# Performance work log

Hardware: AMD Instinct MI355X
Metric: run time of the kernel (lower is better)

## Reference

```python
import jax, jax.numpy as jnp
import numpy as np


def setup_inputs() -> dict:
    key = jax.random.key(0)
    k1, k2 = jax.random.split(key)
    B, T, C = 16, 4096, 128
    unary_logits = jax.random.normal(k1, (B, T, C), dtype=jnp.float32)
    log_trans = jax.random.normal(k2, (C, C), dtype=jnp.float32)
    return {"unary_logits": unary_logits, "log_trans": log_trans}


def reference(unary_logits, log_trans):
    # Row-normalized log transition matrix (log_softmax over dim=1)
    lt = jax.nn.log_softmax(log_trans, axis=1)  # (C, C)
    B, T, C = unary_logits.shape
    u = jnp.swapaxes(unary_logits, 0, 1)  # (T, B, C) time-major for scan

    # Forward recursion: alpha_t = u_t + logsumexp_i(alpha_{t-1}[i] + lt[i, j])
    def fwd_step(a_prev, u_t):
        a_new = u_t + jax.nn.logsumexp(a_prev[:, :, None] + lt[None, :, :], axis=1)
        return a_new, a_new

    a0 = u[0]
    _, alphas_rest = jax.lax.scan(fwd_step, a0, u[1:])
    alpha = jnp.concatenate([a0[None], alphas_rest], axis=0)  # (T, B, C)

    # Backward recursion: beta_t = logsumexp_j(beta_{t+1}[j] + u_{t+1}[j] + lt[i, j])
    def bwd_step(b_next, u_next):
        b_new = jax.nn.logsumexp(
            b_next[:, None, :] + u_next[:, None, :] + lt[None, :, :], axis=2
        )
        return b_new, b_new

    bT = jnp.zeros((B, C), dtype=u.dtype)
    _, betas_rest = jax.lax.scan(bwd_step, bT, u[1:], reverse=True)
    beta = jnp.concatenate([betas_rest, bT[None]], axis=0)  # (T, B, C)

    log_marginals = alpha + beta
    out = jax.nn.log_softmax(log_marginals, axis=-1)
    return jnp.swapaxes(out, 0, 1)  # (B, T, C)
```

## Files before the change

kernel.cpp:

```cpp
#include <hip/hip_runtime.h>
#include <math.h>

#define BB 16
#define TT 4096
#define CC 128

#define LCH 32
#define WCH 48
#define NCH (TT / LCH)

#define ERS 132

typedef float    f32x4  __attribute__((ext_vector_type(4)));
typedef unsigned uint4v __attribute__((ext_vector_type(4)));
typedef __bf16   bf16x8 __attribute__((ext_vector_type(8)));


__device__ __forceinline__ float wave_reduce_max(float v) {
#pragma unroll
    for (int o = 1; o < 64; o <<= 1) v = fmaxf(v, __shfl_xor(v, o, 64));
    return v;
}
__device__ __forceinline__ float wave_reduce_sum(float v) {
#pragma unroll
    for (int o = 1; o < 64; o <<= 1) v += __shfl_xor(v, o, 64);
    return v;
}

__device__ __forceinline__ void lds_barrier() {
    __asm__ __volatile__("s_waitcnt lgkmcnt(0)" ::: "memory");
    __builtin_amdgcn_s_barrier();
}

__device__ __forceinline__ unsigned pkbf(float f) {
    unsigned u = __float_as_uint(f);
    float hi = __uint_as_float(u & 0xffff0000u);
    float lo = f - hi;
    return (u >> 16) | (__float_as_uint(lo) & 0xffff0000u);
}

__global__ __launch_bounds__(CC) void prep_kernel(const float* __restrict__ lt,
                                                  unsigned short* __restrict__ fr) {
    const int r  = blockIdx.x;
    const int j  = threadIdx.x;
    const int wv = j >> 6;
    __shared__ float sm[2];

    float x = lt[r * CC + j];
    float m = wave_reduce_max(x);
    if ((j & 63) == 0) sm[wv] = m;
    __syncthreads();
    m = fmaxf(sm[0], sm[1]);
    __syncthreads();
    float e = __expf(x - m);
    float s = wave_reduce_sum(e);
    if ((j & 63) == 0) sm[wv] = s;
    __syncthreads();
    s = sm[0] + sm[1];
    float p = e / s;

    unsigned pk = pkbf(p);
    unsigned short phi = (unsigned short)(pk & 0xffffu);
    unsigned short plo = (unsigned short)(pk >> 16);

    {
        int T = j >> 4, col = j & 15, kc = r >> 5;
        int ln = (((r & 31) >> 3) << 4) | col, e8 = r & 7;
        size_t o = ((((size_t)(0 * 8 + T) * 4 + kc) * 2 + 0) * 64 + ln) * 8 + e8;
        fr[o] = phi; fr[o + 512] = plo;
    }
    {
        int T = r >> 4, col = r & 15, kc = j >> 5;
        int ln = (((j & 31) >> 3) << 4) | col, e8 = j & 7;
        size_t o = ((((size_t)(1 * 8 + T) * 4 + kc) * 2 + 0) * 64 + ln) * 8 + e8;
        fr[o] = phi; fr[o + 512] = plo;
    }
}

#define BDECL()                                                                \
    bf16x8 Bh_0, Bh_1, Bh_2, Bh_3, Bl_0, Bl_1, Bl_2, Bl_3

#define BLOAD(kc)                                                              \
    do {                                                                       \
        size_t o = ((((size_t)(dirIdx * 8 + wv) * 4 + (kc)) * 2)               \
                        * 64 + lane) * 8;                                      \
        Bh_##kc = __builtin_bit_cast(bf16x8, *(const uint4v*)(fr + o));        \
        Bl_##kc =                                                              \
            __builtin_bit_cast(bf16x8, *(const uint4v*)(fr + o + 512));        \
    } while (0)

#define KC_STEP(kc)                                                            \
    do {                                                                       \
        const uint4v* eptr = (const uint4v*)(epar + arow + (kc) * 32);         \
        uint4v w0 = eptr[0], w1 = eptr[1];                                     \
        uint4v ahw, alw;                                                       \
        ahw.x = __builtin_amdgcn_perm(w0.y, w0.x, 0x05040100u);                \
        ahw.y = __builtin_amdgcn_perm(w0.w, w0.z, 0x05040100u);                \
        ahw.z = __builtin_amdgcn_perm(w1.y, w1.x, 0x05040100u);                \
        ahw.w = __builtin_amdgcn_perm(w1.w, w1.z, 0x05040100u);                \
        alw.x = __builtin_amdgcn_perm(w0.y, w0.x, 0x07060302u);                \
        alw.y = __builtin_amdgcn_perm(w0.w, w0.z, 0x07060302u);                \
        alw.z = __builtin_amdgcn_perm(w1.y, w1.x, 0x07060302u);                \
        alw.w = __builtin_amdgcn_perm(w1.w, w1.z, 0x07060302u);                \
        bf16x8 Ah = __builtin_bit_cast(bf16x8, ahw);                           \
        bf16x8 Al = __builtin_bit_cast(bf16x8, alw);                           \
        accHH = __builtin_amdgcn_mfma_f32_16x16x32_bf16(Ah, Bh_##kc, accHH, 0, 0, 0); \
        accHL = __builtin_amdgcn_mfma_f32_16x16x32_bf16(Ah, Bl_##kc, accHL, 0, 0, 0); \
        accLH = __builtin_amdgcn_mfma_f32_16x16x32_bf16(Al, Bh_##kc, accLH, 0, 0, 0); \
    } while (0)

#define LOADU(d0, ROW)                                                         \
    do {                                                                       \
        size_t ro = (size_t)(ROW) * CC;                                        \
        d0.x = ub0[ro + n1]; d0.y = ub1[ro + n1];                              \
        d0.z = ub2[ro + n1]; d0.w = ub3[ro + n1];                              \
    } while (0)

#define STOREO(s0, ROW)                                                        \
    do {                                                                       \
        size_t ro = (size_t)(ROW) * CC;                                        \
        ob0[ro + n1] = s0.x; ob1[ro + n1] = s0.y;                              \
        ob2[ro + n1] = s0.z; ob3[ro + n1] = s0.w;                              \
    } while (0)

__global__ __launch_bounds__(512, 1)
void scan_kernel(const float* __restrict__ u,
                 const unsigned short* __restrict__ fr,
                 float* __restrict__ alpha,
                 float* __restrict__ beta) {
    const int t    = threadIdx.x;
    const int lane = t & 63;
    const int wv   = t >> 6;
    const int col  = lane & 15;
    const int bb   = (lane >> 4) * 4;
    const int n1   = wv * 16 + col;

    const int  id     = blockIdx.x;
    const bool fwd    = id < NCH;
    const int  c      = fwd ? id : id - NCH;
    const int  dirIdx = fwd ? 0 : 1;

    __shared__ alignas(16) unsigned Epk[2][16 * ERS];
    __shared__ alignas(16) float    wpub[2][16];

    BDECL();
    BLOAD(0); BLOAD(1); BLOAD(2); BLOAD(3);

    const float* ub0 = u + (size_t)(bb + 0) * TT * CC;
    const float* ub1 = u + (size_t)(bb + 1) * TT * CC;
    const float* ub2 = u + (size_t)(bb + 2) * TT * CC;
    const float* ub3 = u + (size_t)(bb + 3) * TT * CC;
    float* obase = fwd ? alpha : beta;
    float* ob0 = obase + (size_t)(bb + 0) * TT * CC;
    float* ob1 = obase + (size_t)(bb + 1) * TT * CC;
    float* ob2 = obase + (size_t)(bb + 2) * TT * CC;
    float* ob3 = obase + (size_t)(bb + 3) * TT * CC;

    const int wlo = c * LCH;
    const int whi = wlo + LCH;
    int t0 = 0, t1 = 0, NS;
    if (fwd) {
        t0 = wlo - WCH; if (t0 < 0) t0 = 0;
        NS = whi - 1 - t0;
    } else {
        t1 = whi - 1 + WCH; if (t1 > TT - 1) t1 = TT - 1;
        NS = t1 - wlo;
    }

    float4 x0, uc0, un0;
    if (fwd) {
        LOADU(x0, t0);
        if (t0 == 0 && wlo == 0) STOREO(x0, 0);
    } else {
        LOADU(x0, t1);
        if (t1 == whi - 1) {
            float4 z4{0.f, 0.f, 0.f, 0.f};
            STOREO(z4, t1);
        }
    }
    {
        int tr0 = fwd ? (t0 + 1) : (t1 - 1);
        LOADU(un0, tr0);
    }
    if (wv == 0 && col == 0) {
        *(float4*)&wpub[0][bb] = x0;
        *(float4*)&wpub[1][bb] = x0;
    }
    lds_barrier();

    const int arow = (lane & 15) * ERS + (lane >> 4) * 8;

    for (int s = 0; s < NS; ++s) {
        const int par = s & 1;
        unsigned* epar = &Epk[par][0];

        float4 wmy = *(const float4*)&wpub[par][bb];
        epar[(bb + 0) * ERS + n1] = pkbf(__expf(x0.x - wmy.x));
        epar[(bb + 1) * ERS + n1] = pkbf(__expf(x0.y - wmy.y));
        epar[(bb + 2) * ERS + n1] = pkbf(__expf(x0.z - wmy.z));
        epar[(bb + 3) * ERS + n1] = pkbf(__expf(x0.w - wmy.w));
        if (wv == 0 && col == 0)
            *(float4*)&wpub[(s + 1) & 1][bb] = x0;

        uc0 = un0;
        int trn = fwd ? (t0 + 2 + s) : (t1 - 2 - s);
        if (trn > TT - 1) trn = TT - 1;
        if (trn < 0) trn = 0;
        LOADU(un0, trn);

        lds_barrier();

        f32x4 accHH = {0.f, 0.f, 0.f, 0.f};
        f32x4 accHL = {0.f, 0.f, 0.f, 0.f};
        f32x4 accLH = {0.f, 0.f, 0.f, 0.f};
        KC_STEP(0); KC_STEP(1); KC_STEP(2); KC_STEP(3);
        f32x4 acc0 = (accHH + accHL) + accLH;

        const int trow = fwd ? (t0 + 1 + s) : (t1 - 1 - s);
        float4 st0;
        if (fwd) {
            st0.x = uc0.x + wmy.x + __logf(acc0.x);
            st0.y = uc0.y + wmy.y + __logf(acc0.y);
            st0.z = uc0.z + wmy.z + __logf(acc0.z);
            st0.w = uc0.w + wmy.w + __logf(acc0.w);
            if (trow >= wlo) STOREO(st0, trow);
            x0 = st0;
        } else {
            st0.x = wmy.x + __logf(acc0.x);
            st0.y = wmy.y + __logf(acc0.y);
            st0.z = wmy.z + __logf(acc0.z);
            st0.w = wmy.w + __logf(acc0.w);
            if (trow < whi) STOREO(st0, trow);
            x0.x = st0.x + uc0.x; x0.y = st0.y + uc0.y;
            x0.z = st0.z + uc0.z; x0.w = st0.w + uc0.w;
        }
    }
}

__global__ __launch_bounds__(256) void combine_kernel(float* __restrict__ out,
                                                      const float* __restrict__ beta) {
    const int    lane = threadIdx.x & 63;
    const int    li   = lane & 31;
    const size_t row  = (size_t)blockIdx.x * 8 + ((threadIdx.x >> 6) << 1) + (lane >> 5);

    float4*       o4 = (float4*)(out + row * CC);
    const float4* b4 = (const float4*)(beta + row * CC);

    float4 a = o4[li];
    float4 bb = b4[li];
    float4 z = float4{a.x + bb.x, a.y + bb.y, a.z + bb.z, a.w + bb.w};

    float m = fmaxf(fmaxf(z.x, z.y), fmaxf(z.z, z.w));
#pragma unroll
    for (int o = 1; o < 32; o <<= 1) m = fmaxf(m, __shfl_xor(m, o, 64));
    float s = __expf(z.x - m) + __expf(z.y - m) + __expf(z.z - m) + __expf(z.w - m);
#pragma unroll
    for (int o = 1; o < 32; o <<= 1) s += __shfl_xor(s, o, 64);
    float ls = m + __logf(s);
    o4[li] = float4{z.x - ls, z.y - ls, z.z - ls, z.w - ls};
}

extern "C" void kernel_launch(void* const* d_in, const int* in_sizes, int n_in,
                              void* d_out, int out_size, void* d_ws, size_t ws_size,
                              hipStream_t stream) {
    const float* u_in = (const float*)d_in[0];
    const float* lt   = (const float*)d_in[1];
    float*       out  = (float*)d_out;

    unsigned short* fr = (unsigned short*)d_ws;
    float* beta = (float*)d_ws + 2 * CC * CC;

    prep_kernel<<<CC, CC, 0, stream>>>(lt, fr);
    scan_kernel<<<2 * NCH, 512, 0, stream>>>(u_in, fr, out, beta);
    combine_kernel<<<(BB * TT) / 8, 256, 0, stream>>>(out, beta);
}
```

Before: 159.6 us.

## Keep scan state in the linear domain and shorten the warmup window

The next step's bf16 exp-weights are now built directly as acc * exp(u + w_prev - w_next), a rescaling of the matmul result. This removes the log-then-exp round trip from the serial dependency chain, and the log is kept only to produce the stored output. A triple-buffered max slot in LDS lets the current and next normalizers be read after the single barrier. The warmup length WCH is also halved, cutting the serial steps per chunk, at the risk of less convergence of the chunked recursion from its arbitrary start state.

Result: faster. 151.8 us (-4.9%).

```diff
diff --git a/kernel.cpp b/kernel.cpp
--- a/kernel.cpp
+++ b/kernel.cpp
@@ -6,7 +6,7 @@
 #define CC 128
 
 #define LCH 32
-#define WCH 48
+#define WCH 24
 #define NCH (TT / LCH)
 
 #define ERS 132
@@ -141,7 +141,7 @@
     const int  dirIdx = fwd ? 0 : 1;
 
     __shared__ alignas(16) unsigned Epk[2][16 * ERS];
-    __shared__ alignas(16) float    wpub[2][16];
+    __shared__ alignas(16) float    wpub[3][16];
 
     BDECL();
     BLOAD(0); BLOAD(1); BLOAD(2); BLOAD(3);
@@ -182,26 +182,31 @@
         int tr0 = fwd ? (t0 + 1) : (t1 - 1);
         LOADU(un0, tr0);
     }
-    if (wv == 0 && col == 0) {
-        *(float4*)&wpub[0][bb] = x0;
-        *(float4*)&wpub[1][bb] = x0;
-    }
+    if (wv == 0 && col == 0) *(float4*)&wpub[0][bb] = x0;
     lds_barrier();
 
     const int arow = (lane & 15) * ERS + (lane >> 4) * 8;
+    unsigned Er0, Er1, Er2, Er3;
+    {
+        float4 w0v = *(const float4*)&wpub[0][bb];
+        Er0 = pkbf(__expf(x0.x - w0v.x));
+        Er1 = pkbf(__expf(x0.y - w0v.y));
+        Er2 = pkbf(__expf(x0.z - w0v.z));
+        Er3 = pkbf(__expf(x0.w - w0v.w));
+        unsigned* e0 = &Epk[0][0];
+        e0[(bb + 0) * ERS + n1] = Er0;
+        e0[(bb + 1) * ERS + n1] = Er1;
+        e0[(bb + 2) * ERS + n1] = Er2;
+        e0[(bb + 3) * ERS + n1] = Er3;
+    }
+    float4 wnv = x0;
+
+    int slc = 0, sln = 1, slx = 2;
 
     for (int s = 0; s < NS; ++s) {
         const int par = s & 1;
-        unsigned* epar = &Epk[par][0];
-
-        float4 wmy = *(const float4*)&wpub[par][bb];
-        epar[(bb + 0) * ERS + n1] = pkbf(__expf(x0.x - wmy.x));
-        epar[(bb + 1) * ERS + n1] = pkbf(__expf(x0.y - wmy.y));
-        epar[(bb + 2) * ERS + n1] = pkbf(__expf(x0.z - wmy.z));
-        epar[(bb + 3) * ERS + n1] = pkbf(__expf(x0.w - wmy.w));
-        if (wv == 0 && col == 0)
-            *(float4*)&wpub[(s + 1) & 1][bb] = x0;
-
+
+        if (wv == 0 && col == 0) *(float4*)&wpub[sln][bb] = wnv;
         uc0 = un0;
         int trn = fwd ? (t0 + 2 + s) : (t1 - 2 - s);
         if (trn > TT - 1) trn = TT - 1;
@@ -210,30 +215,48 @@
 
         lds_barrier();
 
+        unsigned* epar = &Epk[par][0];
+        float4 wmy = *(const float4*)&wpub[slc][bb];
+        float4 wnx = *(const float4*)&wpub[sln][bb];
+        float4 f;
+        f.x = __expf(uc0.x + wmy.x - wnx.x);
+        f.y = __expf(uc0.y + wmy.y - wnx.y);
+        f.z = __expf(uc0.z + wmy.z - wnx.z);
+        f.w = __expf(uc0.w + wmy.w - wnx.w);
+
         f32x4 accHH = {0.f, 0.f, 0.f, 0.f};
         f32x4 accHL = {0.f, 0.f, 0.f, 0.f};
         f32x4 accLH = {0.f, 0.f, 0.f, 0.f};
         KC_STEP(0); KC_STEP(1); KC_STEP(2); KC_STEP(3);
         f32x4 acc0 = (accHH + accHL) + accLH;
 
+        Er0 = pkbf(acc0.x * f.x);
+        Er1 = pkbf(acc0.y * f.y);
+        Er2 = pkbf(acc0.z * f.z);
+        Er3 = pkbf(acc0.w * f.w);
+        unsigned* enx = &Epk[par ^ 1][0];
+        enx[(bb + 0) * ERS + n1] = Er0;
+        enx[(bb + 1) * ERS + n1] = Er1;
+        enx[(bb + 2) * ERS + n1] = Er2;
+        enx[(bb + 3) * ERS + n1] = Er3;
+
         const int trow = fwd ? (t0 + 1 + s) : (t1 - 1 - s);
         float4 st0;
+        st0.x = wmy.x + __logf(acc0.x);
+        st0.y = wmy.y + __logf(acc0.y);
+        st0.z = wmy.z + __logf(acc0.z);
+        st0.w = wmy.w + __logf(acc0.w);
         if (fwd) {
-            st0.x = uc0.x + wmy.x + __logf(acc0.x);
-            st0.y = uc0.y + wmy.y + __logf(acc0.y);
-            st0.z = uc0.z + wmy.z + __logf(acc0.z);
-            st0.w = uc0.w + wmy.w + __logf(acc0.w);
+            st0.x += uc0.x; st0.y += uc0.y; st0.z += uc0.z; st0.w += uc0.w;
             if (trow >= wlo) STOREO(st0, trow);
-            x0 = st0;
+            wnv = st0;
         } else {
-            st0.x = wmy.x + __logf(acc0.x);
-            st0.y = wmy.y + __logf(acc0.y);
-            st0.z = wmy.z + __logf(acc0.z);
-            st0.w = wmy.w + __logf(acc0.w);
             if (trow < whi) STOREO(st0, trow);
-            x0.x = st0.x + uc0.x; x0.y = st0.y + uc0.y;
-            x0.z = st0.z + uc0.z; x0.w = st0.w + uc0.w;
+            wnv.x = st0.x + uc0.x; wnv.y = st0.y + uc0.y;
+            wnv.z = st0.z + uc0.z; wnv.w = st0.w + uc0.w;
         }
+
+        int tmp = slc; slc = sln; sln = slx; slx = tmp;
     }
 }
 
```

## Rescale scan by unary column zero, split bf16 hi/lo LDS, shorten warmup

Applied to the files above, without the earlier changes.

Each step's normaliser is now the input's own column 0 for that row, which is known ahead of time, instead of a value published through LDS from the previous state. The exp-domain state is carried forward as acc*exp(u-u0) with no per-step log/exp round trip. The exp state is stored in separate hi and lo bf16 LDS arrays, so the MFMA operands load directly without perm shuffling. The warmup window is halved, cutting the number of sequential steps per chunk. The trade-offs are that the state is never renormalised to its max, so overflow or underflow is possible, and a shorter warmup may lose accuracy in the chunked approximation.

New measurement: 139.5 us. 12.6% less time.

```diff
diff --git a/kernel.cpp b/kernel.cpp
--- a/kernel.cpp
+++ b/kernel.cpp
@@ -6,10 +6,10 @@
 #define CC 128
 
 #define LCH 32
-#define WCH 48
+#define WCH 24
 #define NCH (TT / LCH)
 
-#define ERS 132
+#define ECS 136
 
 typedef float    f32x4  __attribute__((ext_vector_type(4)));
 typedef unsigned uint4v __attribute__((ext_vector_type(4)));
@@ -91,36 +91,38 @@
 
 #define KC_STEP(kc)                                                            \
     do {                                                                       \
-        const uint4v* eptr = (const uint4v*)(epar + arow + (kc) * 32);         \
-        uint4v w0 = eptr[0], w1 = eptr[1];                                     \
-        uint4v ahw, alw;                                                       \
-        ahw.x = __builtin_amdgcn_perm(w0.y, w0.x, 0x05040100u);                \
-        ahw.y = __builtin_amdgcn_perm(w0.w, w0.z, 0x05040100u);                \
-        ahw.z = __builtin_amdgcn_perm(w1.y, w1.x, 0x05040100u);                \
-        ahw.w = __builtin_amdgcn_perm(w1.w, w1.z, 0x05040100u);                \
-        alw.x = __builtin_amdgcn_perm(w0.y, w0.x, 0x07060302u);                \
-        alw.y = __builtin_amdgcn_perm(w0.w, w0.z, 0x07060302u);                \
-        alw.z = __builtin_amdgcn_perm(w1.y, w1.x, 0x07060302u);                \
-        alw.w = __builtin_amdgcn_perm(w1.w, w1.z, 0x07060302u);                \
-        bf16x8 Ah = __builtin_bit_cast(bf16x8, ahw);                           \
-        bf16x8 Al = __builtin_bit_cast(bf16x8, alw);                           \
+        bf16x8 Ah = __builtin_bit_cast(                                        \
+            bf16x8, *(const uint4v*)(ehp + arow + (kc) * 32));                 \
+        bf16x8 Al = __builtin_bit_cast(                                        \
+            bf16x8, *(const uint4v*)(elp + arow + (kc) * 32));                 \
         accHH = __builtin_amdgcn_mfma_f32_16x16x32_bf16(Ah, Bh_##kc, accHH, 0, 0, 0); \
         accHL = __builtin_amdgcn_mfma_f32_16x16x32_bf16(Ah, Bl_##kc, accHL, 0, 0, 0); \
         accLH = __builtin_amdgcn_mfma_f32_16x16x32_bf16(Al, Bh_##kc, accLH, 0, 0, 0); \
     } while (0)
 
-#define LOADU(d0, ROW)                                                         \
-    do {                                                                       \
-        size_t ro = (size_t)(ROW) * CC;                                        \
-        d0.x = ub0[ro + n1]; d0.y = ub1[ro + n1];                              \
-        d0.z = ub2[ro + n1]; d0.w = ub3[ro + n1];                              \
-    } while (0)
-
-#define STOREO(s0, ROW)                                                        \
-    do {                                                                       \
-        size_t ro = (size_t)(ROW) * CC;                                        \
-        ob0[ro + n1] = s0.x; ob1[ro + n1] = s0.y;                              \
-        ob2[ro + n1] = s0.z; ob3[ro + n1] = s0.w;                              \
+#define LOADU(d0, RO)                                                          \
+    do {                                                                       \
+        d0.x = ub0[(RO) + n1]; d0.y = ub1[(RO) + n1];                          \
+        d0.z = ub2[(RO) + n1]; d0.w = ub3[(RO) + n1];                          \
+    } while (0)
+
+#define LOADW(d0, RO)                                                          \
+    do {                                                                       \
+        d0.x = ub0[(RO)]; d0.y = ub1[(RO)];                                    \
+        d0.z = ub2[(RO)]; d0.w = ub3[(RO)];                                    \
+    } while (0)
+
+#define STOREO(s0, RO)                                                         \
+    do {                                                                       \
+        ob0[(RO) + n1] = s0.x; ob1[(RO) + n1] = s0.y;                          \
+        ob2[(RO) + n1] = s0.z; ob3[(RO) + n1] = s0.w;                          \
+    } while (0)
+
+#define EPUB(dst_h, dst_l, P, I, V)                                            \
+    do {                                                                       \
+        unsigned pk_ = pkbf(V);                                                \
+        dst_h[(bb + I) * ECS + n1] = (unsigned short)pk_;                      \
+        dst_l[(bb + I) * ECS + n1] = (unsigned short)(pk_ >> 16);              \
     } while (0)
 
 __global__ __launch_bounds__(512, 1)
@@ -140,8 +142,8 @@
     const int  c      = fwd ? id : id - NCH;
     const int  dirIdx = fwd ? 0 : 1;
 
-    __shared__ alignas(16) unsigned Epk[2][16 * ERS];
-    __shared__ alignas(16) float    wpub[2][16];
+    __shared__ alignas(16) unsigned short Eh[2][16 * ECS];
+    __shared__ alignas(16) unsigned short El[2][16 * ECS];
 
     BDECL();
     BLOAD(0); BLOAD(1); BLOAD(2); BLOAD(3);
@@ -167,72 +169,80 @@
         NS = t1 - wlo;
     }
 
-    float4 x0, uc0, un0;
+    const int step   = fwd ? CC : -CC;
+    const int roLim  = (TT - 1) * CC;
+    const int wloOff = wlo * CC;
+    const int whiOff = whi * CC;
+
+    int roCur = (fwd ? t0 : t1) * CC;
+
+    float4 x0, d0c;
+    LOADU(x0, roCur); LOADW(d0c, roCur);
     if (fwd) {
-        LOADU(x0, t0);
         if (t0 == 0 && wlo == 0) STOREO(x0, 0);
-    } else {
-        LOADU(x0, t1);
-        if (t1 == whi - 1) {
-            float4 z4{0.f, 0.f, 0.f, 0.f};
-            STOREO(z4, t1);
-        }
+    } else if (t1 == whi - 1) {
+        float4 z4{0.f, 0.f, 0.f, 0.f};
+        STOREO(z4, roCur);
     }
     {
-        int tr0 = fwd ? (t0 + 1) : (t1 - 1);
-        LOADU(un0, tr0);
-    }
-    if (wv == 0 && col == 0) {
-        *(float4*)&wpub[0][bb] = x0;
-        *(float4*)&wpub[1][bb] = x0;
-    }
-    lds_barrier();
-
-    const int arow = (lane & 15) * ERS + (lane >> 4) * 8;
+        unsigned short* eh0 = &Eh[0][0];
+        unsigned short* el0 = &El[0][0];
+        EPUB(eh0, el0, 0, 0, __expf(x0.x - d0c.x));
+        EPUB(eh0, el0, 0, 1, __expf(x0.y - d0c.y));
+        EPUB(eh0, el0, 0, 2, __expf(x0.z - d0c.z));
+        EPUB(eh0, el0, 0, 3, __expf(x0.w - d0c.w));
+    }
+
+    int rpf = roCur + step;
+    float4 un, dn;
+    LOADU(un, rpf); LOADW(dn, rpf);
+
+    const int arow = (lane & 15) * ECS + (lane >> 4) * 8;
 
     for (int s = 0; s < NS; ++s) {
         const int par = s & 1;
-        unsigned* epar = &Epk[par][0];
-
-        float4 wmy = *(const float4*)&wpub[par][bb];
-        epar[(bb + 0) * ERS + n1] = pkbf(__expf(x0.x - wmy.x));
-        epar[(bb + 1) * ERS + n1] = pkbf(__expf(x0.y - wmy.y));
-        epar[(bb + 2) * ERS + n1] = pkbf(__expf(x0.z - wmy.z));
-        epar[(bb + 3) * ERS + n1] = pkbf(__expf(x0.w - wmy.w));
-        if (wv == 0 && col == 0)
-            *(float4*)&wpub[(s + 1) & 1][bb] = x0;
-
-        uc0 = un0;
-        int trn = fwd ? (t0 + 2 + s) : (t1 - 2 - s);
-        if (trn > TT - 1) trn = TT - 1;
-        if (trn < 0) trn = 0;
-        LOADU(un0, trn);
+
+        float4 uc = un, dc = dn;
+        roCur += step;
+        rpf += step;
+        int rc = rpf;
+        if (rc > roLim) rc = roLim;
+        if (rc < 0) rc = 0;
+        LOADU(un, rc); LOADW(dn, rc);
 
         lds_barrier();
 
+        float4 f;
+        f.x = __expf(uc.x - dc.x);
+        f.y = __expf(uc.y - dc.y);
+        f.z = __expf(uc.z - dc.z);
+        f.w = __expf(uc.w - dc.w);
+
+        const unsigned short* ehp = &Eh[par][0];
+        const unsigned short* elp = &El[par][0];
         f32x4 accHH = {0.f, 0.f, 0.f, 0.f};
         f32x4 accHL = {0.f, 0.f, 0.f, 0.f};
         f32x4 accLH = {0.f, 0.f, 0.f, 0.f};
         KC_STEP(0); KC_STEP(1); KC_STEP(2); KC_STEP(3);
         f32x4 acc0 = (accHH + accHL) + accLH;
 
-        const int trow = fwd ? (t0 + 1 + s) : (t1 - 1 - s);
+        unsigned short* ehn = &Eh[par ^ 1][0];
+        unsigned short* eln = &El[par ^ 1][0];
+        EPUB(ehn, eln, 0, 0, acc0.x * f.x);
+        EPUB(ehn, eln, 0, 1, acc0.y * f.y);
+        EPUB(ehn, eln, 0, 2, acc0.z * f.z);
+        EPUB(ehn, eln, 0, 3, acc0.w * f.w);
+
         float4 st0;
+        st0.x = __logf(acc0.x);
+        st0.y = __logf(acc0.y);
+        st0.z = __logf(acc0.z);
+        st0.w = __logf(acc0.w);
         if (fwd) {
-            st0.x = uc0.x + wmy.x + __logf(acc0.x);
-            st0.y = uc0.y + wmy.y + __logf(acc0.y);
-            st0.z = uc0.z + wmy.z + __logf(acc0.z);
-            st0.w = uc0.w + wmy.w + __logf(acc0.w);
-            if (trow >= wlo) STOREO(st0, trow);
-            x0 = st0;
+            st0.x += uc.x; st0.y += uc.y; st0.z += uc.z; st0.w += uc.w;
+            if (roCur >= wloOff) STOREO(st0, roCur);
         } else {
-            st0.x = wmy.x + __logf(acc0.x);
-            st0.y = wmy.y + __logf(acc0.y);
-            st0.z = wmy.z + __logf(acc0.z);
-            st0.w = wmy.w + __logf(acc0.w);
-            if (trow < whi) STOREO(st0, trow);
-            x0.x = st0.x + uc0.x; x0.y = st0.y + uc0.y;
-            x0.z = st0.z + uc0.z; x0.w = st0.w + uc0.w;
+            if (roCur < whiOff) STOREO(st0, roCur);
         }
     }
 }
```
